# Performance work log

Hardware: AMD Instinct MI355X
Metric: run time of the kernel (lower is better)

## Reference

```python
import jax, jax.numpy as jnp
import numpy as np

jax.config.update("jax_enable_x64", True)

# Dims (see shape_source): batch, heads, q-len, kv-len, head-channels, quant group
B, H, T, S, HC = 2, 16, 1024, 1024, 128
G = 8            # group_size from A/R_QUANT_PARAMS
SCALE_SHIFT = 14 # combined dequant shift applied to integer QK scores before softmax
O_SM = 14        # fixed-point offset of the integer softmax output (LUT-style)
PROB_QMAX = 255.0  # 8-bit unsigned probability mantissa (R_QUANT_PARAMS n_bits=8)


def _dequant_po2(q, s):
    """q: int mantissas [..., N], s: nonneg po2 shift exponents [..., N//G].
    Emulates (q << s) per group of G channels (pot_scale activation quantizer)."""
    s_full = jnp.repeat(s, G, axis=-1)
    return q.astype(jnp.float64) * jnp.exp2(s_full.astype(jnp.float64))


def setup_inputs() -> dict:
    key = jax.random.key(0)
    ks = jax.random.split(key, 6)
    # signed 8-bit mantissas in [-128, 127]
    q_q = jax.random.randint(ks[0], (B, H, T, HC), 0, 256, dtype=jnp.int32) - 128
    k_q = jax.random.randint(ks[1], (B, H, S, HC), 0, 256, dtype=jnp.int32) - 128
    vt_q = jax.random.randint(ks[2], (B, H, HC, S), 0, 256, dtype=jnp.int32) - 128
    # nonnegative power-of-two shifts, one per group of G=8
    q_s = jax.random.randint(ks[3], (B, H, T, HC // G), 0, 4, dtype=jnp.int32)
    k_s = jax.random.randint(ks[4], (B, H, S, HC // G), 0, 4, dtype=jnp.int32)
    vt_s = jax.random.randint(ks[5], (B, H, HC, S // G), 0, 4, dtype=jnp.int32)
    return {"q_q": q_q, "q_s": q_s, "k_q": k_q, "k_s": k_s, "vt_q": vt_q, "vt_s": vt_s}


def reference(q_q, q_s, k_q, k_s, vt_q, vt_s):
    # ---- shift_qk_matmul: (q_q << q_s) @ (k_q << k_s)^T in float64, truncated to int64
    q = _dequant_po2(q_q, q_s)                       # [B,H,T,HC] f64
    k = _dequant_po2(k_q, k_s)                       # [B,H,S,HC] f64
    scores = jnp.einsum("bhtc,bhsc->bhts", q, k).astype(jnp.int64)

    # ---- integer softmax emulation: rescale integer scores, softmax, then
    # re-quantize probabilities with an 8-bit per-group (G=8 along S) po2 scale
    logits = scores.astype(jnp.float32) * np.float32(2.0 ** (-SCALE_SHIFT) / np.sqrt(HC))
    p = jax.nn.softmax(logits, axis=-1)              # [B,H,T,S]
    val = jnp.round(p * (2.0 ** O_SM))               # fixed-point probs (ints)
    vg = val.reshape(B, H, T, S // G, G)
    gmax = jnp.max(vg, axis=-1, keepdims=True)
    r_shift = jnp.clip(jnp.ceil(jnp.log2(jnp.maximum(gmax, 1.0) / PROB_QMAX)), 0.0, None)
    r_q = jnp.clip(jnp.round(vg / jnp.exp2(r_shift)), 0.0, PROB_QMAX)
    r = (r_q * jnp.exp2(r_shift)).reshape(B, H, T, S).astype(jnp.float64)  # (r_q << r_s)

    # ---- shift_rv_matmul: r @ (vt_q << vt_s)^T in float64, truncated to int64
    vt = _dequant_po2(vt_q, vt_s)                    # [B,H,HC,S] f64
    a = jnp.einsum("bhts,bhcs->bhtc", r, vt).astype(jnp.int64)  # [B,H,T,HC]
    return a
```

## Files before the change

### kernel.cpp

```cpp
#include <hip/hip_runtime.h>
#include <string.h>


typedef int   v4i __attribute__((ext_vector_type(4)));
typedef float v4f __attribute__((ext_vector_type(4)));
typedef short v8s __attribute__((ext_vector_type(8)));

#define BHN 32
#define TN  1024
#define SN  1024
#define HCN 128
#define TT  16
#define RST 1032
#define KD_BH 262144
#define VD_BH 262144
#define WS_NEED ((size_t)BHN*(KD_BH+VD_BH))

__device__ __forceinline__ unsigned pack_b(int b0,int b1,int b2,int b3){
    return (unsigned)((b0&255)|((b1&255)<<8)|((b2&255)<<16)|((b3&255)<<24));
}

__device__ __forceinline__ void dig16(const int* __restrict__ p, int s0, int s1,
                                      v4i& hi, v4i& lo){
    #pragma unroll
    for (int wi=0; wi<4; ++wi){
        v4i m = *(const v4i*)(p + wi*4);
        int s = (wi<2) ? s0 : s1;
        int d0=m[0]<<s, d1=m[1]<<s, d2=m[2]<<s, d3=m[3]<<s;
        hi[wi] = (int)pack_b(d0>>4,d1>>4,d2>>4,d3>>4);
        lo[wi] = (int)pack_b(d0&15,d1&15,d2&15,d3&15);
    }
}

__device__ __forceinline__ unsigned short bf16_of_int(int v){
    return (unsigned short)(__float_as_uint((float)v) >> 16);
}

__global__ __launch_bounds__(256) void digitize(
    const int* __restrict__ k_q, const int* __restrict__ k_s,
    const int* __restrict__ vt_q, const int* __restrict__ vt_s,
    unsigned char* __restrict__ kd, unsigned char* __restrict__ vd)
{
    const int w    = threadIdx.x >> 6;
    const int lane = threadIdx.x & 63;
    const int l15  = lane & 15;
    const int task = blockIdx.x*4 + w;
    if (task < 4096){
        const int kc = task & 1, n = (task>>1)&7, ch = (task>>4)&7, bh = task>>7;
        const int q4   = lane >> 4;
        const int srow = bh*SN + ch*128 + n*16 + l15;
        const int gb   = srow*16 + kc*8 + q4*2;
        v4i hi, lo;
        dig16(k_q + (size_t)srow*HCN + kc*64 + q4*16, k_s[gb], k_s[gb+1], hi, lo);
        size_t base = (size_t)bh*KD_BH + (size_t)(ch*32768 + n*4096 + kc*2048 + lane*16);
        *(v4i*)(kd + base)        = hi;
        *(v4i*)(kd + base + 1024) = lo;
    } else {
        const int t  = task - 4096;
        const int n  = t & 7, kb = (t>>3)&31, bh = t>>8;
        const int sub = lane >> 4;
        const int row = bh*HCN + n*16 + l15;
        const int* vp = vt_q + (size_t)row*SN + kb*32 + sub*8;
        const int s   = vt_s[row*128 + kb*4 + sub];
        unsigned wds[4];
        #pragma unroll
        for (int j=0;j<4;j++){
            int a = vp[j*2]   << s;
            int b = vp[j*2+1] << s;
            wds[j] = (unsigned)bf16_of_int(a) | ((unsigned)bf16_of_int(b) << 16);
        }
        size_t base = (size_t)bh*VD_BH + (size_t)(((kb*8 + n)*64 + lane)*16);
        *(v4i*)(vd + base) = v4i{(int)wds[0],(int)wds[1],(int)wds[2],(int)wds[3]};
    }
}

template<bool PK>
__global__ __launch_bounds__(256,4) void mha_mfma(
    const int* __restrict__ q_q, const int* __restrict__ q_s,
    const int* __restrict__ k_q, const int* __restrict__ k_s,
    const int* __restrict__ vt_q, const int* __restrict__ vt_s,
    const unsigned char* __restrict__ kd, const unsigned char* __restrict__ vd,
    int* __restrict__ out)
{
    __shared__ __align__(16) unsigned short rbuf[16*RST];
    __shared__ float red[128];

    const int tid  = threadIdx.x;
    const int ln   = tid & 15;
    const int qd4  = (tid >> 4) & 3;
    const int w    = tid >> 6;
    const int lane = tid & 63;
    const int blk = blockIdx.x;
    const int bh  = ((blk>>9)<<3) | (blk&7);
    const int t0  = ((blk>>3)&63) * TT;

    v4i qfh[2], qfl[2];
    {
        const int* qrow  = q_q + (size_t)(bh*TN + t0 + ln)*HCN;
        const int* qsrow = q_s + (size_t)(bh*TN + t0 + ln)*16;
        #pragma unroll
        for (int kc=0; kc<2; ++kc){
            int gi = kc*8 + qd4*2;
            dig16(qrow + kc*64 + qd4*16, qsrow[gi], qsrow[gi+1], qfh[kc], qfl[kc]);
        }
    }

    int scv[16][4];

    const v4i* kb_ = (const v4i*)(kd + (size_t)bh*KD_BH);
    for (int ch=0; ch<8; ++ch){
        #pragma unroll
        for (int i=0;i<2;i++){
            const int n = w*2 + i;
            v4i a2{0,0,0,0}, a1{0,0,0,0}, a0{0,0,0,0};
            #pragma unroll
            for (int kc=0;kc<2;kc++){
                v4i bhv, blv;
                if (PK){
                    const v4i* tb = kb_ + (ch*8+n)*256 + kc*128 + lane;
                    bhv = tb[0];
                    blv = tb[64];
                } else {
                    int srow = bh*SN + ch*128 + n*16 + ln;
                    int cc   = kc*64 + qd4*16;
                    dig16(k_q + (size_t)srow*128 + cc,
                          k_s[srow*16 + (cc>>3)], k_s[srow*16 + (cc>>3) + 1], bhv, blv);
                }
                a2 = __builtin_amdgcn_mfma_i32_16x16x64_i8(qfh[kc], bhv, a2, 0,0,0);
                a1 = __builtin_amdgcn_mfma_i32_16x16x64_i8(qfl[kc], bhv, a1, 0,0,0);
                a1 = __builtin_amdgcn_mfma_i32_16x16x64_i8(qfh[kc], blv, a1, 0,0,0);
                a0 = __builtin_amdgcn_mfma_i32_16x16x64_i8(qfl[kc], blv, a0, 0,0,0);
            }
            int st = ch*2 + i;
            #pragma unroll
            for (int r=0;r<4;r++)
                scv[st][r] = (a2[r]<<8) + (a1[r]<<4) + a0[r];
        }
    }

    const float CS2 = (float)(6.103515625e-05 / 11.313708498984760390566
                              * 1.4426950408889634074);
    float mx[4];
    #pragma unroll
    for (int r=0;r<4;r++){
        float m_ = -3.0e38f;
        #pragma unroll
        for (int st=0;st<16;st++){
            float f = (float)scv[st][r] * CS2;
            scv[st][r] = __float_as_int(f);
            m_ = fmaxf(m_, f);
        }
        #pragma unroll
        for (int o=8;o>0;o>>=1) m_ = fmaxf(m_, __shfl_xor(m_, o));
        mx[r] = m_;
    }
    if (ln == 0){
        #pragma unroll
        for (int r=0;r<4;r++) red[w*16 + qd4*4 + r] = mx[r];
    }
    __syncthreads();
    float sm[4];
    #pragma unroll
    for (int r=0;r<4;r++){
        float m_ = fmaxf(fmaxf(red[qd4*4+r], red[16+qd4*4+r]),
                         fmaxf(red[32+qd4*4+r], red[48+qd4*4+r]));
        float s_ = 0.f;
        #pragma unroll
        for (int st=0;st<16;st++){
            float t = __int_as_float(scv[st][r]) - m_;
            float e;
            asm("v_exp_f32 %0, %1" : "=v"(e) : "v"(t));
            scv[st][r] = __float_as_int(e);
            s_ += e;
        }
        #pragma unroll
        for (int o=8;o>0;o>>=1) s_ += __shfl_xor(s_, o);
        sm[r] = s_;
    }
    if (ln == 0){
        #pragma unroll
        for (int r=0;r<4;r++) red[64 + w*16 + qd4*4 + r] = sm[r];
    }
    __syncthreads();
    float inv14[4];
    #pragma unroll
    for (int r=0;r<4;r++){
        float s_ = red[64+qd4*4+r] + red[80+qd4*4+r] + red[96+qd4*4+r] + red[112+qd4*4+r];
        inv14[r] = 16384.0f / s_;
    }

    #pragma unroll
    for (int st=0;st<16;st++){
        int colb = (st>>1)*128 + (w*2+(st&1))*16;
        #pragma unroll
        for (int r=0;r<4;r++){
            int val = (int)rintf(__int_as_float(scv[st][r]) * inv14[r]);
            int row = qd4*4 + r;
            int col = colb + ln;
            int gs  = (col>>3) ^ (row&7);
            rbuf[row*RST + gs*8 + (col&7)] = (unsigned short)val;
        }
    }
    __syncthreads();

    {
        const int prow = tid >> 4;
        const int pc   = tid & 15;
        unsigned short* rp = rbuf + prow*RST;
        #pragma unroll
        for (int i=0;i<8;i++){
            const int cg  = pc + 16*i;
            const int off = (cg ^ (prow & 7)) << 3;
            v8s v = *(const v8s*)(rp + off);
            int g01 = max((int)v[0], (int)v[1]), g23 = max((int)v[2], (int)v[3]);
            int g45 = max((int)v[4], (int)v[5]), g67 = max((int)v[6], (int)v[7]);
            int gmax = max(max(g01, g23), max(g45, g67));
            int gi = max(gmax, 1);
            int x  = gi - 1;
            int e2 = 31 - __clz(x | 255);
            int sh = (e2 - 7) + ((x >> (e2 - 7)) == 255);
            float isc = __int_as_float((127 - sh) << 23);
            v8s o;
            #pragma unroll
            for (int j=0;j<8;j++){
                float rq = fminf(rintf((float)(int)v[j] * isc), 255.0f);
                o[j] = (short)bf16_of_int(((int)rq) << sh);
            }
            *(v8s*)(rp + off) = o;
        }
    }
    __syncthreads();

    const v4i* vb = (const v4i*)(vd + (size_t)bh*VD_BH);
    v4f acc0{0,0,0,0}, acc1{0,0,0,0};
    #pragma unroll 4
    for (int kb=0; kb<32; ++kb){
        v8s af = *(const v8s*)(rbuf + ln*RST + (((kb*4+qd4) ^ (ln&7))<<3));
        v4i b0, b1;
        if (PK){
            b0 = vb[(kb*8 + w*2    )*64 + lane];
            b1 = vb[(kb*8 + w*2 + 1)*64 + lane];
        } else {
            #pragma unroll
            for (int i=0;i<2;i++){
                int chan = (w*2+i)*16 + ln;
                const int* vp = vt_q + (size_t)(bh*HCN + chan)*SN + kb*32 + qd4*8;
                int s = vt_s[(bh*HCN + chan)*128 + kb*4 + qd4];
                unsigned wd[4];
                #pragma unroll
                for (int j=0;j<4;j++){
                    int a = vp[j*2]   << s;
                    int b = vp[j*2+1] << s;
                    wd[j] = (unsigned)bf16_of_int(a) | ((unsigned)bf16_of_int(b)<<16);
                }
                v4i t{(int)wd[0],(int)wd[1],(int)wd[2],(int)wd[3]};
                if (i==0) b0 = t; else b1 = t;
            }
        }
        v8s bs0, bs1;
        memcpy(&bs0, &b0, 16);
        memcpy(&bs1, &b1, 16);
        acc0 = __builtin_amdgcn_mfma_f32_16x16x32_bf16(af, bs0, acc0, 0,0,0);
        acc1 = __builtin_amdgcn_mfma_f32_16x16x32_bf16(af, bs1, acc1, 0,0,0);
    }
    #pragma unroll
    for (int r=0;r<4;r++){
        size_t o = (size_t)(bh*TN + t0 + qd4*4 + r)*HCN + (w*2)*16 + ln;
        out[o]      = (int)rintf(acc0[r]);
        out[o + 16] = (int)rintf(acc1[r]);
    }
}

extern "C" void kernel_launch(void* const* d_in, const int* in_sizes, int n_in,
                              void* d_out, int out_size, void* d_ws, size_t ws_size,
                              hipStream_t stream) {
    const int* q_q  = (const int*)d_in[0];
    const int* q_s  = (const int*)d_in[1];
    const int* k_q  = (const int*)d_in[2];
    const int* k_s  = (const int*)d_in[3];
    const int* vt_q = (const int*)d_in[4];
    const int* vt_s = (const int*)d_in[5];
    int* out = (int*)d_out;

    unsigned char* kd = (unsigned char*)d_ws;
    unsigned char* vd = kd + (size_t)BHN*KD_BH;

    if (ws_size >= WS_NEED){
        digitize<<<dim3(3072), 256, 0, stream>>>(k_q,k_s,vt_q,vt_s, kd,vd);
        mha_mfma<true><<<dim3(2048), 256, 0, stream>>>(
            q_q,q_s,k_q,k_s,vt_q,vt_s, kd,vd, out);
    } else {
        mha_mfma<false><<<dim3(2048), 256, 0, stream>>>(
            q_q,q_s,k_q,k_s,vt_q,vt_s, kd,vd, out);
    }
}
```

Measured before the change: 156.4 us.

## Transpose QK MFMA operands so rows map to lanes; fuse prob requant in registers

Swaps the A/B operands of the int8 QK MFMAs, so each lane now holds four consecutive key columns of one query row instead of four rows. With that layout, the row max and sum reductions need only two cross-lane shuffles, and the per-group (8 columns) max for probability requantization comes from one shuffle. The separate LDS write, barrier and re-read pass for requantization is removed. Probabilities are converted to bf16 and packed with v_perm, then stored as 8-byte vectors using a new swizzle. The extra barrier and the scalar 2-byte LDS stores go away, at the cost of a more intricate swizzle that has to stay consistent with the PV-stage reads.

After: 151.8 us. 3.0% less time.

```diff
diff --git a/kernel.cpp b/kernel.cpp
--- a/kernel.cpp
+++ b/kernel.cpp
@@ -5,6 +5,7 @@
 typedef int   v4i __attribute__((ext_vector_type(4)));
 typedef float v4f __attribute__((ext_vector_type(4)));
 typedef short v8s __attribute__((ext_vector_type(8)));
+typedef unsigned v2u __attribute__((ext_vector_type(2)));
 
 #define BHN 32
 #define TN  1024
@@ -126,10 +127,10 @@
                     dig16(k_q + (size_t)srow*128 + cc,
                           k_s[srow*16 + (cc>>3)], k_s[srow*16 + (cc>>3) + 1], bhv, blv);
                 }
-                a2 = __builtin_amdgcn_mfma_i32_16x16x64_i8(qfh[kc], bhv, a2, 0,0,0);
-                a1 = __builtin_amdgcn_mfma_i32_16x16x64_i8(qfl[kc], bhv, a1, 0,0,0);
-                a1 = __builtin_amdgcn_mfma_i32_16x16x64_i8(qfh[kc], blv, a1, 0,0,0);
-                a0 = __builtin_amdgcn_mfma_i32_16x16x64_i8(qfl[kc], blv, a0, 0,0,0);
+                a2 = __builtin_amdgcn_mfma_i32_16x16x64_i8(bhv, qfh[kc], a2, 0,0,0);
+                a1 = __builtin_amdgcn_mfma_i32_16x16x64_i8(bhv, qfl[kc], a1, 0,0,0);
+                a1 = __builtin_amdgcn_mfma_i32_16x16x64_i8(blv, qfh[kc], a1, 0,0,0);
+                a0 = __builtin_amdgcn_mfma_i32_16x16x64_i8(blv, qfl[kc], a0, 0,0,0);
             }
             int st = ch*2 + i;
             #pragma unroll
@@ -140,102 +141,85 @@
 
     const float CS2 = (float)(6.103515625e-05 / 11.313708498984760390566
                               * 1.4426950408889634074);
-    float mx[4];
-    #pragma unroll
-    for (int r=0;r<4;r++){
-        float m_ = -3.0e38f;
+    {
+        float m0=-3.0e38f, m1=-3.0e38f, m2=-3.0e38f, m3=-3.0e38f;
         #pragma unroll
         for (int st=0;st<16;st++){
-            float f = (float)scv[st][r] * CS2;
-            scv[st][r] = __float_as_int(f);
-            m_ = fmaxf(m_, f);
-        }
-        #pragma unroll
-        for (int o=8;o>0;o>>=1) m_ = fmaxf(m_, __shfl_xor(m_, o));
-        mx[r] = m_;
-    }
-    if (ln == 0){
-        #pragma unroll
-        for (int r=0;r<4;r++) red[w*16 + qd4*4 + r] = mx[r];
+            float f0 = (float)scv[st][0]*CS2; scv[st][0]=__float_as_int(f0); m0=fmaxf(m0,f0);
+            float f1 = (float)scv[st][1]*CS2; scv[st][1]=__float_as_int(f1); m1=fmaxf(m1,f1);
+            float f2 = (float)scv[st][2]*CS2; scv[st][2]=__float_as_int(f2); m2=fmaxf(m2,f2);
+            float f3 = (float)scv[st][3]*CS2; scv[st][3]=__float_as_int(f3); m3=fmaxf(m3,f3);
+        }
+        float m_ = fmaxf(fmaxf(m0,m1), fmaxf(m2,m3));
+        m_ = fmaxf(m_, __shfl_xor(m_, 16));
+        m_ = fmaxf(m_, __shfl_xor(m_, 32));
+        if ((tid & 48) == 0) red[w*16 + ln] = m_;
     }
     __syncthreads();
-    float sm[4];
-    #pragma unroll
-    for (int r=0;r<4;r++){
-        float m_ = fmaxf(fmaxf(red[qd4*4+r], red[16+qd4*4+r]),
-                         fmaxf(red[32+qd4*4+r], red[48+qd4*4+r]));
-        float s_ = 0.f;
+    const float mrow = fmaxf(fmaxf(red[ln], red[16+ln]), fmaxf(red[32+ln], red[48+ln]));
+    float inv14;
+    {
+        float s0=0.f, s1=0.f, s2=0.f, s3=0.f;
         #pragma unroll
         for (int st=0;st<16;st++){
-            float t = __int_as_float(scv[st][r]) - m_;
-            float e;
-            asm("v_exp_f32 %0, %1" : "=v"(e) : "v"(t));
-            scv[st][r] = __float_as_int(e);
-            s_ += e;
-        }
-        #pragma unroll
-        for (int o=8;o>0;o>>=1) s_ += __shfl_xor(s_, o);
-        sm[r] = s_;
-    }
-    if (ln == 0){
-        #pragma unroll
-        for (int r=0;r<4;r++) red[64 + w*16 + qd4*4 + r] = sm[r];
+            #pragma unroll
+            for (int r=0;r<4;r++){
+                float t_ = __int_as_float(scv[st][r]) - mrow;
+                float e;
+                asm("v_exp_f32 %0, %1" : "=v"(e) : "v"(t_));
+                scv[st][r] = __float_as_int(e);
+                if (r==0) s0 += e; else if (r==1) s1 += e; else if (r==2) s2 += e; else s3 += e;
+            }
+        }
+        float s_ = (s0+s1) + (s2+s3);
+        s_ += __shfl_xor(s_, 16);
+        s_ += __shfl_xor(s_, 32);
+        if ((tid & 48) == 0) red[64 + w*16 + ln] = s_;
     }
     __syncthreads();
-    float inv14[4];
-    #pragma unroll
-    for (int r=0;r<4;r++){
-        float s_ = red[64+qd4*4+r] + red[80+qd4*4+r] + red[96+qd4*4+r] + red[112+qd4*4+r];
-        inv14[r] = 16384.0f / s_;
-    }
-
-    #pragma unroll
-    for (int st=0;st<16;st++){
-        int colb = (st>>1)*128 + (w*2+(st&1))*16;
-        #pragma unroll
-        for (int r=0;r<4;r++){
-            int val = (int)rintf(__int_as_float(scv[st][r]) * inv14[r]);
-            int row = qd4*4 + r;
-            int col = colb + ln;
-            int gs  = (col>>3) ^ (row&7);
-            rbuf[row*RST + gs*8 + (col&7)] = (unsigned short)val;
-        }
-    }
-    __syncthreads();
-
-    {
-        const int prow = tid >> 4;
-        const int pc   = tid & 15;
-        unsigned short* rp = rbuf + prow*RST;
-        #pragma unroll
-        for (int i=0;i<8;i++){
-            const int cg  = pc + 16*i;
-            const int off = (cg ^ (prow & 7)) << 3;
-            v8s v = *(const v8s*)(rp + off);
-            int g01 = max((int)v[0], (int)v[1]), g23 = max((int)v[2], (int)v[3]);
-            int g45 = max((int)v[4], (int)v[5]), g67 = max((int)v[6], (int)v[7]);
-            int gmax = max(max(g01, g23), max(g45, g67));
-            int gi = max(gmax, 1);
+    {
+        float sum = red[64+ln] + red[80+ln] + red[96+ln] + red[112+ln];
+        inv14 = 16384.0f / sum;
+    }
+
+    {
+        unsigned short* rp = rbuf + ln*RST;
+        const int swzr = (ln & 7) ^ ((ln & 8) >> 1);
+        const int cbase = (w*2)*16 + qd4*4;
+        #pragma unroll
+        for (int st=0;st<16;st++){
+            float v0 = rintf(__int_as_float(scv[st][0]) * inv14);
+            float v1 = rintf(__int_as_float(scv[st][1]) * inv14);
+            float v2 = rintf(__int_as_float(scv[st][2]) * inv14);
+            float v3 = rintf(__int_as_float(scv[st][3]) * inv14);
+            float g = fmaxf(fmaxf(v0,v1), fmaxf(v2,v3));
+            g = fmaxf(g, __shfl_xor(g, 16));
+            int gi = max((int)g, 1);
             int x  = gi - 1;
             int e2 = 31 - __clz(x | 255);
             int sh = (e2 - 7) + ((x >> (e2 - 7)) == 255);
             float isc = __int_as_float((127 - sh) << 23);
-            v8s o;
-            #pragma unroll
-            for (int j=0;j<8;j++){
-                float rq = fminf(rintf((float)(int)v[j] * isc), 255.0f);
-                o[j] = (short)bf16_of_int(((int)rq) << sh);
-            }
-            *(v8s*)(rp + off) = o;
+            float fsc = __int_as_float((127 + sh) << 23);
+            unsigned b0 = __float_as_uint(rintf(v0*isc) * fsc);
+            unsigned b1 = __float_as_uint(rintf(v1*isc) * fsc);
+            unsigned b2 = __float_as_uint(rintf(v2*isc) * fsc);
+            unsigned b3 = __float_as_uint(rintf(v3*isc) * fsc);
+            unsigned w0 = __builtin_amdgcn_perm(b1, b0, 0x07060302u);
+            unsigned w1 = __builtin_amdgcn_perm(b3, b2, 0x07060302u);
+            int c0 = ((st>>1)*128) + cbase + ((st&1)*16);
+            int gs = (c0>>3) ^ swzr;
+            *(v2u*)(rp + gs*8 + (c0&7)) = v2u{w0, w1};
         }
     }
     __syncthreads();
 
     const v4i* vb = (const v4i*)(vd + (size_t)bh*VD_BH);
+    const unsigned short* rp2 = rbuf + ln*RST;
+    const int swzr2 = (ln & 7) ^ ((ln & 8) >> 1);
     v4f acc0{0,0,0,0}, acc1{0,0,0,0};
     #pragma unroll 4
     for (int kb=0; kb<32; ++kb){
-        v8s af = *(const v8s*)(rbuf + ln*RST + (((kb*4+qd4) ^ (ln&7))<<3));
+        v8s af = *(const v8s*)(rp2 + (((kb*4+qd4) ^ swzr2) << 3));
         v4i b0, b1;
         if (PK){
             b0 = vb[(kb*8 + w*2    )*64 + lane];
```
